# Performance work log

Measured on AMD Instinct MI355X. Metric: run time of the kernel, lower is better.

The kernel has to match this reference:

```python
import jax, jax.numpy as jnp
import numpy as np

B, S, E, W = 16, 1024, 1024, 7  # batch, seq_len, emb_dim, (odd) window size
PAD_VAL = 0.0  # padding_idx used as constant pad value in the torch code


def setup_inputs() -> dict:
    key = jax.random.key(0)
    kx, kw, kb = jax.random.split(key, 3)
    x = jax.random.normal(kx, (B, S, E), dtype=jnp.float32)
    # per-position Linear(E*W -> W): torch default init U(-1/sqrt(fan_in), 1/sqrt(fan_in))
    bound = 1.0 / np.sqrt(W * E)
    weight = jax.random.uniform(kw, (S, W, W * E), minval=-bound, maxval=bound, dtype=jnp.float32)
    bias = jax.random.uniform(kb, (S, W), minval=-bound, maxval=bound, dtype=jnp.float32)
    return {"x": x, "weight": weight, "bias": bias}


def reference(x, weight, bias):
    Bb, Ss, Ee = x.shape
    Wn = bias.shape[1]
    hw = Wn // 2
    # constant-pad the sequence dim with padding_idx value
    padded = jnp.pad(x, ((0, 0), (hw, hw), (0, 0)), constant_values=PAD_VAL)
    # gather all windows at once: windows[b, t, w, e] = padded[b, t + w, e]
    idx = jnp.arange(Ss)[:, None] + jnp.arange(Wn)[None, :]  # [S, W]
    windows = padded[:, idx, :]  # [B, S, W, E]
    # per-position linear on flattened window: weight[t] is [W_out=W, W*E]
    w4 = weight.reshape(Ss, Wn, Wn, Ee)  # [t, v, w, e]
    logits = jnp.einsum('btwe,tvwe->btv', windows, w4) + bias[None, :, :]  # [B, S, W]
    gates = jax.nn.sigmoid(logits)
    # gated sum over window, then tanh
    out = jnp.tanh(jnp.einsum('btw,btwe->bte', gates, windows))  # [B, S, E]
    return out
```

## Files before the change

### kernel.cpp

```cpp
#include <hip/hip_runtime.h>


#define Bq 16
#define Sq 1024
#define Eq 1024
#define Wq 7
#define HWq 3

__global__ __launch_bounds__(256, 4) void soft_reorder_kernel(
    const float* __restrict__ x,
    const float* __restrict__ weight,
    const float* __restrict__ bias,
    float* __restrict__ out)
{
    const int bid = blockIdx.x;
    const int t = (bid & 7) * (Sq / 8) + (bid >> 3);
    const int tid = threadIdx.x;
    const int b = tid >> 4;
    const int j = tid & 15;

    __shared__ float gates[Bq][Wq + 1];

    const float* wt = weight + (size_t)t * (Wq * Wq * Eq);

    float4 acc[Wq];
#pragma unroll
    for (int v = 0; v < Wq; ++v) acc[v] = make_float4(0.f, 0.f, 0.f, 0.f);

#pragma unroll
    for (int w = 0; w < Wq; ++w) {
        const int row = t + w - HWq;
        if ((unsigned)row < (unsigned)Sq) {
            const float* xr = x + ((size_t)b * Sq + row) * Eq;
            const float* wr = wt + w * Eq;
            for (int ee = j * 4; ee < Eq; ee += 64) {
                const float4 xv = *(const float4*)(xr + ee);
#pragma unroll
                for (int v = 0; v < Wq; ++v) {
                    const float4 wv = *(const float4*)(wr + (size_t)v * (Wq * Eq) + ee);
                    acc[v].x += xv.x * wv.x;
                    acc[v].y += xv.y * wv.y;
                    acc[v].z += xv.z * wv.z;
                    acc[v].w += xv.w * wv.w;
                }
            }
        }
    }

#pragma unroll
    for (int v = 0; v < Wq; ++v) {
        float s = acc[v].x + acc[v].y + acc[v].z + acc[v].w;
        s += __shfl_xor(s, 1, 16);
        s += __shfl_xor(s, 2, 16);
        s += __shfl_xor(s, 4, 16);
        s += __shfl_xor(s, 8, 16);
        if (j == 0) {
            const float logit = s + bias[t * Wq + v];
            gates[b][v] = 1.0f / (1.0f + __expf(-logit));
        }
    }
    __syncthreads();

    const int e = tid * 4;
    for (int bb = 0; bb < Bq; ++bb) {
        float g[Wq];
#pragma unroll
        for (int w = 0; w < Wq; ++w) g[w] = gates[bb][w];

        float4 a = make_float4(0.f, 0.f, 0.f, 0.f);
#pragma unroll
        for (int w = 0; w < Wq; ++w) {
            const int row = t + w - HWq;
            if ((unsigned)row < (unsigned)Sq) {
                const float4 xv = *(const float4*)(x + ((size_t)bb * Sq + row) * Eq + e);
                a.x += g[w] * xv.x;
                a.y += g[w] * xv.y;
                a.z += g[w] * xv.z;
                a.w += g[w] * xv.w;
            }
        }
        float4 o;
        o.x = 1.0f - 2.0f / (1.0f + __expf(2.0f * a.x));
        o.y = 1.0f - 2.0f / (1.0f + __expf(2.0f * a.y));
        o.z = 1.0f - 2.0f / (1.0f + __expf(2.0f * a.z));
        o.w = 1.0f - 2.0f / (1.0f + __expf(2.0f * a.w));
        *(float4*)(out + ((size_t)bb * Sq + t) * Eq + e) = o;
    }
}

extern "C" void kernel_launch(void* const* d_in, const int* in_sizes, int n_in,
                              void* d_out, int out_size, void* d_ws, size_t ws_size,
                              hipStream_t stream) {
    const float* x = (const float*)d_in[0];
    const float* weight = (const float*)d_in[1];
    const float* bias = (const float*)d_in[2];
    float* out = (float*)d_out;

    soft_reorder_kernel<<<Sq, 256, 0, stream>>>(x, weight, bias, out);
}
```

Measured before the change: 476.9 us.

## Quadruple block size and split embedding reduction across four thread chunks

Each block now uses 1024 threads instead of 256. In the logits phase each quarter of the block covers one quarter of the embedding dimension, and the partial dot products are combined through shared memory before the sigmoid. In the output phase each quarter handles four batches instead of one thread looping over all sixteen. This adds parallelism and memory-level concurrency per block, at the cost of an extra shared-memory reduction step, an extra barrier, and possible register-pressure limits at 1024 threads.

```diff
diff --git a/kernel.cpp b/kernel.cpp
--- a/kernel.cpp
+++ b/kernel.cpp
@@ -6,8 +6,10 @@
 #define Eq 1024
 #define Wq 7
 #define HWq 3
+#define WE (Wq * Eq)
+#define WWE (Wq * WE)
 
-__global__ __launch_bounds__(256, 4) void soft_reorder_kernel(
+__global__ __launch_bounds__(1024, 8) void soft_reorder_kernel(
     const float* __restrict__ x,
     const float* __restrict__ weight,
     const float* __restrict__ bias,
@@ -16,12 +18,15 @@
     const int bid = blockIdx.x;
     const int t = (bid & 7) * (Sq / 8) + (bid >> 3);
     const int tid = threadIdx.x;
-    const int b = tid >> 4;
     const int j = tid & 15;
+    const int b = (tid >> 4) & 15;
+    const int chunk = tid >> 8;
+    const int ebase = chunk * 256 + j * 4;
 
+    __shared__ float partial[Bq][4][Wq];
     __shared__ float gates[Bq][Wq + 1];
 
-    const float* wt = weight + (size_t)t * (Wq * Wq * Eq);
+    const float* wt = weight + (size_t)t * WWE;
 
     float4 acc[Wq];
 #pragma unroll
@@ -33,11 +38,13 @@
         if ((unsigned)row < (unsigned)Sq) {
             const float* xr = x + ((size_t)b * Sq + row) * Eq;
             const float* wr = wt + w * Eq;
-            for (int ee = j * 4; ee < Eq; ee += 64) {
+#pragma unroll
+            for (int s = 0; s < 4; ++s) {
+                const int ee = ebase + s * 64;
                 const float4 xv = *(const float4*)(xr + ee);
 #pragma unroll
                 for (int v = 0; v < Wq; ++v) {
-                    const float4 wv = *(const float4*)(wr + (size_t)v * (Wq * Eq) + ee);
+                    const float4 wv = *(const float4*)(wr + (size_t)v * WE + ee);
                     acc[v].x += xv.x * wv.x;
                     acc[v].y += xv.y * wv.y;
                     acc[v].z += xv.z * wv.z;
@@ -54,15 +61,24 @@
         s += __shfl_xor(s, 2, 16);
         s += __shfl_xor(s, 4, 16);
         s += __shfl_xor(s, 8, 16);
-        if (j == 0) {
-            const float logit = s + bias[t * Wq + v];
-            gates[b][v] = 1.0f / (1.0f + __expf(-logit));
-        }
+        if (j == 0) partial[b][chunk][v] = s;
     }
     __syncthreads();
 
-    const int e = tid * 4;
-    for (int bb = 0; bb < Bq; ++bb) {
+    if (tid < Bq * Wq) {
+        const int bb = tid / Wq;
+        const int v = tid - bb * Wq;
+        const float s = partial[bb][0][v] + partial[bb][1][v] +
+                        partial[bb][2][v] + partial[bb][3][v] + bias[t * Wq + v];
+        gates[bb][v] = 1.0f / (1.0f + __expf(-s));
+    }
+    __syncthreads();
+
+    const int e = (tid & 255) * 4;
+    const int bq = tid >> 8;
+#pragma unroll
+    for (int k = 0; k < 4; ++k) {
+        const int bb = bq * 4 + k;
         float g[Wq];
 #pragma unroll
         for (int w = 0; w < Wq; ++w) g[w] = gates[bb][w];
@@ -96,5 +112,5 @@
     const float* bias = (const float*)d_in[2];
     float* out = (float*)d_out;
 
-    soft_reorder_kernel<<<Sq, 256, 0, stream>>>(x, weight, bias, out);
+    soft_reorder_kernel<<<Sq, 1024, 0, stream>>>(x, weight, bias, out);
 }
```

After: 872.8 us. +83.0%, slower.
